# Performance work log

Measured on AMD Instinct MI355X. Metric: run time of the kernel, lower is better.

## Reference

```python
import jax, jax.numpy as jnp
import numpy as np

H = 256      # hidden_dim
NH = 4       # num_heads
DK = H // NH # per-head dim
NL = 2       # num self-attn layers
TL = 6       # transformer_num_layers (output repeat)
PTS_DIM = 3


def _layer_norm(x, g, b, eps=1e-5):
    m = jnp.mean(x, axis=-1, keepdims=True)
    v = jnp.mean((x - m) ** 2, axis=-1, keepdims=True)
    return (x - m) / jnp.sqrt(v + eps) * g + b


def _mha(x, Wq, bq, Wk, bk, Wv, bv, Wo, bo, g, bb, bias):
    # x: [B,N,H]; bias: [B,NH,N,N]; way='add' (att_spm_type='add')
    B, N, _ = x.shape
    q = (x @ Wq + bq).reshape(B, N, NH, DK).transpose(0, 2, 1, 3)  # [B,h,N,d]
    k = (x @ Wk + bk).reshape(B, N, NH, DK).transpose(0, 2, 1, 3)
    v = (x @ Wv + bv).reshape(B, N, NH, DK).transpose(0, 2, 1, 3)
    att = jnp.einsum('bhnd,bhmd->bhnm', q, k) / np.sqrt(DK).astype(np.float32)
    att = jax.nn.softmax(att + bias, axis=-1)
    out = jnp.einsum('bhnm,bhmd->bhnd', att, v).transpose(0, 2, 1, 3).reshape(B, N, H)
    out = out @ Wo + bo
    return _layer_norm(x + out, g, bb)


def setup_inputs() -> dict:
    key = jax.random.key(0)
    ks = jax.random.split(key, 16)
    B, N = 1, 512
    s = 0.02  # weight init scale
    inp = {
        'history_states': jax.random.normal(ks[0], (TL, B, N, H), jnp.float32),
        'all_lanes_preds': jax.random.normal(ks[1], (TL, B, N, 33), jnp.float32),
        'fc_W': jax.random.normal(ks[2], (H, H), jnp.float32) * s,
        'fc_b': jnp.zeros((H,), jnp.float32),
        'Wq': jax.random.normal(ks[3], (NL, H, H), jnp.float32) * s,
        'bq': jnp.zeros((NL, H), jnp.float32),
        'Wk': jax.random.normal(ks[4], (NL, H, H), jnp.float32) * s,
        'bk': jnp.zeros((NL, H), jnp.float32),
        'Wv': jax.random.normal(ks[5], (NL, H, H), jnp.float32) * s,
        'bv': jnp.zeros((NL, H), jnp.float32),
        'Wo': jax.random.normal(ks[6], (NL, H, H), jnp.float32) * s,
        'bo': jnp.zeros((NL, H), jnp.float32),
        'ln_g': jnp.ones((NL, H), jnp.float32),
        'ln_b': jnp.zeros((NL, H), jnp.float32),
        'mlp1_W': jax.random.normal(ks[7], (H, H), jnp.float32) * s,
        'mlp1_b': jnp.zeros((H,), jnp.float32),
        'mlp2_W': jax.random.normal(ks[8], (H, H), jnp.float32) * s,
        'mlp2_b': jnp.zeros((H,), jnp.float32),
        'cls_W1': jax.random.normal(ks[9], (2 * H, H), jnp.float32) * s,
        'cls_b1': jnp.zeros((H,), jnp.float32),
        'cls_W2': jax.random.normal(ks[10], (H, 1), jnp.float32) * s,
        'cls_b2': jnp.zeros((1,), jnp.float32),
    }
    return inp


def reference(history_states, all_lanes_preds, fc_W, fc_b, Wq, bq, Wk, bk, Wv, bv,
              Wo, bo, ln_g, ln_b, mlp1_W, mlp1_b, mlp2_W, mlp2_b,
              cls_W1, cls_b1, cls_W2, cls_b2):
    query_feats = history_states[-1]                 # [B,N,H]
    coords = all_lanes_preds[-1]                      # [B,N,33]
    B, N, C = coords.shape
    coords = coords.reshape(B, N, C // PTS_DIM, PTS_DIM)
    query_end_point = coords[:, :, -1, :]             # [B,N,3]
    key_start_point = coords[:, :, 0, :]              # [B,N,3]

    # pairwise distance bias: dist[b,i,j] = ||key_start[j] - query_end[i]||
    diff = key_start_point[:, None, :, :] - query_end_point[:, :, None, :]
    dist = jnp.sqrt(jnp.sum(diff ** 2, axis=-1))[:, None, :, :]  # [B,1,N,N]
    dw = 1.0 / (dist + 0.01)
    dw = dw / jnp.sum(dw, axis=2, keepdims=True)      # normalize over dim 2
    zeros = jnp.zeros_like(dw)
    dist_weights = jax.lax.stop_gradient(
        jnp.concatenate([dw, -dist, zeros, zeros], axis=1))  # [B,4,N,N]

    # features_concat: Linear + ReLU
    x = jax.nn.relu(query_feats @ fc_W + fc_b)

    for i in range(NL):
        x = _mha(x, Wq[i], bq[i], Wk[i], bk[i], Wv[i], bv[i],
                 Wo[i], bo[i], ln_g[i], ln_b[i], dist_weights)

    # lclc relationship head: per-side MLP, pairwise concat, classifier
    o1 = jax.nn.relu(x @ mlp1_W + mlp1_b)             # [B,N,H]
    o2 = jax.nn.relu(x @ mlp2_W + mlp2_b)
    pair = jnp.concatenate([
        jnp.broadcast_to(o1[:, :, None, :], (B, N, N, H)),
        jnp.broadcast_to(o2[:, None, :, :], (B, N, N, H))], axis=-1)  # [B,N,N,2H]
    z = jax.nn.relu(pair @ cls_W1 + cls_b1)
    lclc = (z @ cls_W2 + cls_b2)[..., 0]              # [B,N,N]
    all_lclc_preds = jnp.broadcast_to(lclc[None], (TL, B, N, N))
    return all_lclc_preds
```

## Files before the change

### kernel.cpp

```cpp
#include <hip/hip_runtime.h>
#include <math.h>


#define NTOK 512
#define HDIM 256
#define DKH  64
#define NHEAD 4
#define TLEN 6
#define WSZ  65536
#define PSTR 520
#define XPS  264

typedef __attribute__((ext_vector_type(8))) short bf16x8;
typedef __attribute__((ext_vector_type(4))) float f32x4;

__device__ __forceinline__ ushort f2bf(float f)
{
    unsigned u = __builtin_bit_cast(unsigned, f);
    u += 0x7FFFu + ((u >> 16) & 1u);
    return (ushort)(u >> 16);
}
__device__ __forceinline__ float bf_lo(unsigned u)
{
    return __builtin_bit_cast(float, u << 16);
}
__device__ __forceinline__ float bf_hi(unsigned u)
{
    return __builtin_bit_cast(float, u & 0xFFFF0000u);
}

struct PKArg {
    const float* w[13];
    const float* pl;
    ushort* wpk;
    float *dist, *dwraw, *inv_cs;
};

__global__ __launch_bounds__(256) void pack_kernel(PKArg p)
{
    __shared__ __align__(16) ushort smu[64 * 72];
    const int bid = blockIdx.x;
    const int t   = threadIdx.x;

    if (bid < 208) {
        const int mat  = bid >> 4;
        const int tile = bid & 15;
        const int k0   = (tile >> 2) * 64;
        const int c0   = (tile & 3) * 64;
        const float* W = p.w[mat];
#pragma unroll
        for (int j = 0; j < 4; ++j) {
            const int i  = t + j * 256;
            const int r  = i >> 4, c4 = i & 15;
            const float4 v4 = *(const float4*)&W[(k0 + r) * HDIM + c0 + c4 * 4];
            smu[(c4 * 4 + 0) * 72 + r] = f2bf(v4.x);
            smu[(c4 * 4 + 1) * 72 + r] = f2bf(v4.y);
            smu[(c4 * 4 + 2) * 72 + r] = f2bf(v4.z);
            smu[(c4 * 4 + 3) * 72 + r] = f2bf(v4.w);
        }
        __syncthreads();
#pragma unroll
        for (int j = 0; j < 2; ++j) {
            const int i  = t + j * 256;
            const int cr = i >> 3, kk = i & 7;
            const uint4 v = *(const uint4*)&smu[cr * 72 + kk * 8];
            *(uint4*)&p.wpk[mat * WSZ + (c0 + cr) * HDIM + k0 + kk * 8] = v;
        }
    } else {
        float* smf = (float*)smu;
        float* qe  = smf;
        float* red = smf + 1536;
        const int item = bid - 208;
        for (int i = t; i < 512; i += 256) {
            qe[i * 3 + 0] = p.pl[i * 33 + 30];
            qe[i * 3 + 1] = p.pl[i * 33 + 31];
            qe[i * 3 + 2] = p.pl[i * 33 + 32];
        }
        __syncthreads();
        const int m   = item * 64 + (t & 63);
        const int nch = t >> 6;
        const float kx = p.pl[m * 33 + 0], ky = p.pl[m * 33 + 1], kz = p.pl[m * 33 + 2];
        float cs = 0.f;
        for (int n = nch * 128; n < nch * 128 + 128; ++n) {
            const float dx = kx - qe[n * 3 + 0];
            const float dy = ky - qe[n * 3 + 1];
            const float dz = kz - qe[n * 3 + 2];
            const float dd = sqrtf(dx * dx + dy * dy + dz * dz);
            const float w  = 1.0f / (dd + 0.01f);
            p.dist[n * NTOK + m]  = dd;
            p.dwraw[n * NTOK + m] = w;
            cs += w;
        }
        red[nch * 64 + (t & 63)] = cs;
        __syncthreads();
        if (t < 64)
            p.inv_cs[item * 64 + t] =
                1.0f / (red[t] + red[64 + t] + red[128 + t] + red[192 + t]);
    }
}

__device__ __forceinline__ void qkv_one2(
    const ushort* __restrict__ xpan, const ushort* __restrict__ Wt,
    const float* __restrict__ bb, int prob,
    int slab, int c0, int lr, int lg, int lk,
    ushort* __restrict__ q16, ushort* __restrict__ k16,
    ushort* __restrict__ vT16)
{
    const ushort* Ap = xpan + lr * XPS + lk;
    f32x4 acc[2];
    acc[0] = (f32x4){0.f, 0.f, 0.f, 0.f};
    acc[1] = (f32x4){0.f, 0.f, 0.f, 0.f};
#pragma unroll
    for (int ks = 0; ks < 8; ++ks) {
        const bf16x8 a = *(const bf16x8*)&Ap[ks * 32];
#pragma unroll
        for (int j = 0; j < 2; ++j) {
            const bf16x8 b = *(const bf16x8*)&Wt[(c0 + j * 16 + lr) * HDIM + ks * 32 + lk];
            acc[j] = __builtin_amdgcn_mfma_f32_16x16x32_bf16(a, b, acc[j], 0, 0, 0);
        }
    }
#pragma unroll
    for (int j = 0; j < 2; ++j) {
        const int col = c0 + j * 16 + lr;
        const float bv2 = bb[col];
        if (prob < 2) {
            ushort* dst = (prob == 0) ? q16 : k16;
#pragma unroll
            for (int rg = 0; rg < 4; ++rg)
                dst[(slab + lg * 4 + rg) * HDIM + col] = f2bf(acc[j][rg] + bv2);
        } else {
            ushort4 s = {f2bf(acc[j][0] + bv2), f2bf(acc[j][1] + bv2),
                         f2bf(acc[j][2] + bv2), f2bf(acc[j][3] + bv2)};
            *(ushort4*)&vT16[col * NTOK + slab + lg * 4] = s;
        }
    }
}

__global__ __launch_bounds__(256) void fcqkv(
    const float* __restrict__ qf, const ushort* __restrict__ fcWt,
    const float* __restrict__ fcb,
    const ushort* __restrict__ WqT, const float* __restrict__ bq,
    const ushort* __restrict__ WkT, const float* __restrict__ bk,
    const ushort* __restrict__ WvT, const float* __restrict__ bv,
    float* __restrict__ xa, ushort* __restrict__ q16,
    ushort* __restrict__ k16, ushort* __restrict__ vT16)
{
    __shared__ __align__(16) ushort xpan[16 * XPS];
    const int bid  = blockIdx.x;
    const int p6   = bid >> 5;
    const int slab = (bid & 31) * 16;
    const int t = threadIdx.x;
    const int wv = t >> 6, lane = t & 63;
    const int lr = lane & 15, lg = lane >> 4, lk = lg * 8;
    const int c0 = wv * 64;

    {
        f32x4 acc[4];
#pragma unroll
        for (int j = 0; j < 4; ++j) acc[j] = (f32x4){0.f, 0.f, 0.f, 0.f};
        const float* Aq = qf + (slab + lr) * HDIM + lk;
#pragma unroll
        for (int ks = 0; ks < 8; ++ks) {
            const float4 a0 = *(const float4*)&Aq[ks * 32];
            const float4 a1 = *(const float4*)&Aq[ks * 32 + 4];
            bf16x8 a;
            a[0] = (short)f2bf(a0.x); a[1] = (short)f2bf(a0.y);
            a[2] = (short)f2bf(a0.z); a[3] = (short)f2bf(a0.w);
            a[4] = (short)f2bf(a1.x); a[5] = (short)f2bf(a1.y);
            a[6] = (short)f2bf(a1.z); a[7] = (short)f2bf(a1.w);
#pragma unroll
            for (int j = 0; j < 4; ++j) {
                const bf16x8 b = *(const bf16x8*)&fcWt[(c0 + j * 16 + lr) * HDIM + ks * 32 + lk];
                acc[j] = __builtin_amdgcn_mfma_f32_16x16x32_bf16(a, b, acc[j], 0, 0, 0);
            }
        }
#pragma unroll
        for (int j = 0; j < 4; ++j) {
            const int col = c0 + j * 16 + lr;
            const float bbv = fcb[col];
#pragma unroll
            for (int rg = 0; rg < 4; ++rg) {
                const float o = fmaxf(acc[j][rg] + bbv, 0.f);
                if (p6 == 0) xa[(slab + lg * 4 + rg) * HDIM + col] = o;
                xpan[(lg * 4 + rg) * XPS + col] = f2bf(o);
            }
        }
    }
    __syncthreads();
    const int prob = p6 >> 1, ch = p6 & 1;
    const ushort* Wt = (prob == 0) ? WqT : (prob == 1) ? WkT : WvT;
    const float*  bb = (prob == 0) ? bq  : (prob == 1) ? bk  : bv;
    qkv_one2(xpan, Wt, bb, prob, slab, ch * 128 + wv * 32, lr, lg, lk,
             q16, k16, vT16);
}

__global__ __launch_bounds__(512) void attn_fused(
    const ushort* __restrict__ q16, const ushort* __restrict__ k16,
    const ushort* __restrict__ vT16, const float* __restrict__ dist,
    const float* __restrict__ dwraw, const float* __restrict__ inv_cs,
    ushort* __restrict__ ao16)
{
    __shared__ __align__(16) ushort P_lds[16 * PSTR];
    __shared__ __align__(16) float exch[2][16][64];
    __shared__ float rmax[8][16];
    __shared__ float psums[8][16];

    const int bid = blockIdx.x;
    const int h  = bid >> 5;
    const int n0 = (bid & 31) * 16;
    const int t  = threadIdx.x;
    const int wv = t >> 6, lane = t & 63;
    const int lr = lane & 15, lg = lane >> 4, lk = lg * 8;
    const int mW = wv * 64;

    const ushort* Qrow = q16 + (n0 + lr) * HDIM + h * DKH + lk;
    const bf16x8 a0 = *(const bf16x8*)&Qrow[0];
    const bf16x8 a1 = *(const bf16x8*)&Qrow[32];

    f32x4 accs[4];
#pragma unroll
    for (int cg = 0; cg < 4; ++cg) accs[cg] = (f32x4){0.f, 0.f, 0.f, 0.f};
#pragma unroll
    for (int cg = 0; cg < 4; ++cg) {
        const ushort* Brow = k16 + (mW + cg * 16 + lr) * HDIM + h * DKH + lk;
        accs[cg] = __builtin_amdgcn_mfma_f32_16x16x32_bf16(
            a0, *(const bf16x8*)&Brow[0], accs[cg], 0, 0, 0);
        accs[cg] = __builtin_amdgcn_mfma_f32_16x16x32_bf16(
            a1, *(const bf16x8*)&Brow[32], accs[cg], 0, 0, 0);
    }

    const int db = wv & 3, kh = wv >> 2;
    const ushort* Vrow = vT16 + (h * DKH + db * 16 + lr) * NTOK + kh * 256 + lk;
    bf16x8 vfrag[8];
#pragma unroll
    for (int c = 0; c < 8; ++c)
        vfrag[c] = *(const bf16x8*)&Vrow[c * 32];

    float s[4][4];
#pragma unroll
    for (int cg = 0; cg < 4; ++cg) {
        const int m = mW + cg * 16 + lr;
        const float ic = (h == 0) ? inv_cs[m] : 0.f;
#pragma unroll
        for (int rg = 0; rg < 4; ++rg) {
            const int n = n0 + lg * 4 + rg;
            float b = 0.f;
            if (h == 0)      b = dwraw[n * NTOK + m] * ic;
            else if (h == 1) b = -dist[n * NTOK + m];
            s[cg][rg] = accs[cg][rg] * 0.125f + b;
        }
    }

    float mx[4];
#pragma unroll
    for (int rg = 0; rg < 4; ++rg) {
        float m = fmaxf(fmaxf(s[0][rg], s[1][rg]), fmaxf(s[2][rg], s[3][rg]));
#pragma unroll
        for (int o = 1; o < 16; o <<= 1) m = fmaxf(m, __shfl_xor(m, o));
        mx[rg] = m;
    }
    if (lr == 0)
#pragma unroll
        for (int rg = 0; rg < 4; ++rg) rmax[wv][lg * 4 + rg] = mx[rg];
    __syncthreads();
    float mxf[4];
#pragma unroll
    for (int rg = 0; rg < 4; ++rg) {
        const int row = lg * 4 + rg;
        float m = rmax[0][row];
#pragma unroll
        for (int w = 1; w < 8; ++w) m = fmaxf(m, rmax[w][row]);
        mxf[rg] = m;
    }

    float ps[4] = {0.f, 0.f, 0.f, 0.f};
#pragma unroll
    for (int cg = 0; cg < 4; ++cg)
#pragma unroll
        for (int rg = 0; rg < 4; ++rg) {
            const float e = __expf(s[cg][rg] - mxf[rg]);
            ps[rg] += e;
            P_lds[(lg * 4 + rg) * PSTR + mW + cg * 16 + lr] = f2bf(e);
        }
#pragma unroll
    for (int rg = 0; rg < 4; ++rg) {
#pragma unroll
        for (int o = 1; o < 16; o <<= 1) ps[rg] += __shfl_xor(ps[rg], o);
    }
    if (lr == 0)
#pragma unroll
        for (int rg = 0; rg < 4; ++rg) psums[wv][lg * 4 + rg] = ps[rg];
    __syncthreads();

    {
        f32x4 acco = (f32x4){0.f, 0.f, 0.f, 0.f};
        const ushort* Prow = P_lds + lr * PSTR + kh * 256 + lk;
#pragma unroll
        for (int c = 0; c < 8; ++c) {
            const bf16x8 pa = *(const bf16x8*)&Prow[c * 32];
            acco = __builtin_amdgcn_mfma_f32_16x16x32_bf16(pa, vfrag[c], acco, 0, 0, 0);
        }
#pragma unroll
        for (int rg = 0; rg < 4; ++rg)
            exch[kh][lg * 4 + rg][db * 16 + lr] = acco[rg];
    }
    __syncthreads();

    if (t < 256) {
        const int r = t >> 4, d4 = t & 15;
        f32x4 sum = *(const f32x4*)&exch[0][r][d4 * 4];
        sum += *(const f32x4*)&exch[1][r][d4 * 4];
        float den = 0.f;
#pragma unroll
        for (int w = 0; w < 8; ++w) den += psums[w][r];
        const float inv = 1.0f / den;
        ushort4 o = {f2bf(sum.x * inv), f2bf(sum.y * inv),
                     f2bf(sum.z * inv), f2bf(sum.w * inv)};
        *(ushort4*)&ao16[(n0 + r) * HDIM + h * DKH + d4 * 4] = o;
    }
}

__device__ __forceinline__ void oprojln_phase(
    const ushort* __restrict__ ao16, const ushort* __restrict__ WoT,
    const float* __restrict__ bo, const float* __restrict__ gamma,
    const float* __restrict__ beta, const float* __restrict__ x,
    int slab, int c0, int wv, int lr, int lg, int lk,
    float red[4][16], f32x4 acc[4])
{
    const ushort* Arow = ao16 + (slab + lr) * HDIM + lk;
#pragma unroll
    for (int j = 0; j < 4; ++j) acc[j] = (f32x4){0.f, 0.f, 0.f, 0.f};
#pragma unroll
    for (int ks = 0; ks < 8; ++ks) {
        const bf16x8 a = *(const bf16x8*)&Arow[ks * 32];
#pragma unroll
        for (int j = 0; j < 4; ++j) {
            const bf16x8 b = *(const bf16x8*)&WoT[(c0 + j * 16 + lr) * HDIM + ks * 32 + lk];
            acc[j] = __builtin_amdgcn_mfma_f32_16x16x32_bf16(a, b, acc[j], 0, 0, 0);
        }
    }
#pragma unroll
    for (int j = 0; j < 4; ++j) {
        const int col = c0 + j * 16 + lr;
        const float bc = bo[col];
#pragma unroll
        for (int rg = 0; rg < 4; ++rg)
            acc[j][rg] += bc + x[(slab + lg * 4 + rg) * HDIM + col];
    }

    float sm[4];
#pragma unroll
    for (int rg = 0; rg < 4; ++rg) {
        float s = 0.f;
#pragma unroll
        for (int j = 0; j < 4; ++j) s += acc[j][rg];
#pragma unroll
        for (int o = 1; o < 16; o <<= 1) s += __shfl_xor(s, o);
        sm[rg] = s;
    }
    if (lr == 0)
#pragma unroll
        for (int rg = 0; rg < 4; ++rg) red[wv][lg * 4 + rg] = sm[rg];
    __syncthreads();
    float mean[4];
#pragma unroll
    for (int rg = 0; rg < 4; ++rg) {
        const int row = lg * 4 + rg;
        mean[rg] = (red[0][row] + red[1][row] + red[2][row] + red[3][row]) * (1.f / 256.f);
    }
    __syncthreads();

#pragma unroll
    for (int rg = 0; rg < 4; ++rg) {
        float s2 = 0.f;
#pragma unroll
        for (int j = 0; j < 4; ++j) {
            const float c = acc[j][rg] - mean[rg];
            s2 += c * c;
        }
#pragma unroll
        for (int o = 1; o < 16; o <<= 1) s2 += __shfl_xor(s2, o);
        sm[rg] = s2;
    }
    if (lr == 0)
#pragma unroll
        for (int rg = 0; rg < 4; ++rg) red[wv][lg * 4 + rg] = sm[rg];
    __syncthreads();
    float rstd[4];
#pragma unroll
    for (int rg = 0; rg < 4; ++rg) {
        const int row = lg * 4 + rg;
        const float var = (red[0][row] + red[1][row] + red[2][row] + red[3][row]) * (1.f / 256.f);
        rstd[rg] = rsqrtf(var + 1e-5f);
    }
#pragma unroll
    for (int j = 0; j < 4; ++j) {
        const int col = c0 + j * 16 + lr;
        const float gg = gamma[col], bv = beta[col];
#pragma unroll
        for (int rg = 0; rg < 4; ++rg)
            acc[j][rg] = (acc[j][rg] - mean[rg]) * rstd[rg] * gg + bv;
    }
}

__global__ __launch_bounds__(256) void oprojqkv(
    const ushort* __restrict__ ao16, const ushort* __restrict__ WoT,
    const float* __restrict__ bo, const float* __restrict__ gamma,
    const float* __restrict__ beta,
    const ushort* __restrict__ WqT, const float* __restrict__ bq,
    const ushort* __restrict__ WkT, const float* __restrict__ bk,
    const ushort* __restrict__ WvT, const float* __restrict__ bv,
    const float* __restrict__ xa, float* __restrict__ xb,
    ushort* __restrict__ q16, ushort* __restrict__ k16,
    ushort* __restrict__ vT16)
{
    __shared__ __align__(16) ushort xpan[16 * XPS];
    __shared__ float red[4][16];
    const int bid  = blockIdx.x;
    const int p6   = bid >> 5;
    const int slab = (bid & 31) * 16;
    const int t = threadIdx.x;
    const int wv = t >> 6, lane = t & 63;
    const int lr = lane & 15, lg = lane >> 4, lk = lg * 8;
    const int c0 = wv * 64;

    f32x4 acc[4];
    oprojln_phase(ao16, WoT, bo, gamma, beta, xa, slab, c0, wv, lr, lg, lk, red, acc);
#pragma unroll
    for (int j = 0; j < 4; ++j) {
        const int col = c0 + j * 16 + lr;
#pragma unroll
        for (int rg = 0; rg < 4; ++rg) {
            if (p6 == 0) xb[(slab + lg * 4 + rg) * HDIM + col] = acc[j][rg];
            xpan[(lg * 4 + rg) * XPS + col] = f2bf(acc[j][rg]);
        }
    }
    __syncthreads();
    const int prob = p6 >> 1, ch = p6 & 1;
    const ushort* Wt = (prob == 0) ? WqT : (prob == 1) ? WkT : WvT;
    const float*  bb = (prob == 0) ? bq  : (prob == 1) ? bk  : bv;
    qkv_one2(xpan, Wt, bb, prob, slab, ch * 128 + wv * 32, lr, lg, lk,
             q16, k16, vT16);
}

__global__ __launch_bounds__(256) void oprojmlpU(
    const ushort* __restrict__ ao16, const ushort* __restrict__ WoT,
    const float* __restrict__ bo, const float* __restrict__ gamma,
    const float* __restrict__ beta,
    const ushort* __restrict__ m1WT, const float* __restrict__ m1b,
    const ushort* __restrict__ m2WT, const float* __restrict__ m2b,
    const ushort* __restrict__ cW1aT, const float* __restrict__ cb1,
    const ushort* __restrict__ cW1bT,
    const float* __restrict__ xb, ushort* __restrict__ U1b,
    ushort* __restrict__ U2b)
{
    __shared__ __align__(16) ushort xpan[16 * XPS];
    __shared__ __align__(16) ushort opan[16 * XPS];
    __shared__ float red[4][16];
    const int bid  = blockIdx.x;
    const int p4   = bid >> 5;
    const int p    = p4 >> 1, ch = p4 & 1;
    const int slab = (bid & 31) * 16;
    const int t = threadIdx.x;
    const int wv = t >> 6, lane = t & 63;
    const int lr = lane & 15, lg = lane >> 4, lk = lg * 8;
    const int c0 = wv * 64;

    f32x4 acc[4];
    oprojln_phase(ao16, WoT, bo, gamma, beta, xb, slab, c0, wv, lr, lg, lk, red, acc);
#pragma unroll
    for (int j = 0; j < 4; ++j) {
        const int col = c0 + j * 16 + lr;
#pragma unroll
        for (int rg = 0; rg < 4; ++rg)
            xpan[(lg * 4 + rg) * XPS + col] = f2bf(acc[j][rg]);
    }
    __syncthreads();

    {
        const ushort* Wt = p ? m2WT : m1WT;
        const float*  bb = p ? m2b  : m1b;
        const ushort* Ap = xpan + lr * XPS + lk;
        f32x4 a2[4];
#pragma unroll
        for (int j = 0; j < 4; ++j) a2[j] = (f32x4){0.f, 0.f, 0.f, 0.f};
#pragma unroll
        for (int ks = 0; ks < 8; ++ks) {
            const bf16x8 a = *(const bf16x8*)&Ap[ks * 32];
#pragma unroll
            for (int j = 0; j < 4; ++j) {
                const bf16x8 b = *(const bf16x8*)&Wt[(c0 + j * 16 + lr) * HDIM + ks * 32 + lk];
                a2[j] = __builtin_amdgcn_mfma_f32_16x16x32_bf16(a, b, a2[j], 0, 0, 0);
            }
        }
#pragma unroll
        for (int j = 0; j < 4; ++j) {
            const int col = c0 + j * 16 + lr;
            const float bbv = bb[col];
#pragma unroll
            for (int rg = 0; rg < 4; ++rg)
                opan[(lg * 4 + rg) * XPS + col] = f2bf(fmaxf(a2[j][rg] + bbv, 0.f));
        }
    }
    __syncthreads();

    {
        const ushort* Wt = p ? cW1bT : cW1aT;
        ushort* U        = p ? U2b : U1b;
        const int cb     = ch * 128 + wv * 32;
        const ushort* Ao = opan + lr * XPS + lk;
        f32x4 a2[2];
        a2[0] = (f32x4){0.f, 0.f, 0.f, 0.f};
        a2[1] = (f32x4){0.f, 0.f, 0.f, 0.f};
#pragma unroll
        for (int ks = 0; ks < 8; ++ks) {
            const bf16x8 a = *(const bf16x8*)&Ao[ks * 32];
#pragma unroll
            for (int j = 0; j < 2; ++j) {
                const bf16x8 b = *(const bf16x8*)&Wt[(cb + j * 16 + lr) * HDIM + ks * 32 + lk];
                a2[j] = __builtin_amdgcn_mfma_f32_16x16x32_bf16(a, b, a2[j], 0, 0, 0);
            }
        }
#pragma unroll
        for (int j = 0; j < 2; ++j) {
            const int col = cb + j * 16 + lr;
            const float bbv = (p == 0) ? cb1[col] : 0.f;
#pragma unroll
            for (int rg = 0; rg < 4; ++rg)
                U[(slab + lg * 4 + rg) * HDIM + col] = f2bf(a2[j][rg] + bbv);
        }
    }
}

__global__ __launch_bounds__(256) void pair_cls(const ushort* __restrict__ U1b,
                                                const ushort* __restrict__ U2b,
                                                const float* __restrict__ W2,
                                                const float* __restrict__ b2,
                                                float* __restrict__ out)
{
    __shared__ __align__(16) ushort u1s[32][264];
    __shared__ __align__(16) ushort u2s[32][264];
    __shared__ __align__(16) float w2s[256];
    const int t  = threadIdx.x;
    const int n0 = blockIdx.y * 32, m0 = blockIdx.x * 32;

#pragma unroll
    for (int u = 0; u < 4; ++u) {
        const int i = t + u * 256;
        const int r = i >> 5, c8 = i & 31;
        *(uint4*)&u1s[r][c8 * 8] = *(const uint4*)&U1b[(n0 + r) * HDIM + c8 * 8];
        *(uint4*)&u2s[r][c8 * 8] = *(const uint4*)&U2b[(m0 + r) * HDIM + c8 * 8];
    }
    if (t < 64) *(float4*)&w2s[t * 4] = *(const float4*)&W2[t * 4];
    __syncthreads();

    const int tx = t & 15, ty = t >> 4;
    const ushort* r0 = &u1s[ty * 2][0];
    const ushort* r1 = &u1s[ty * 2 + 1][0];
    const ushort* c0 = &u2s[tx * 2][0];
    const ushort* c1 = &u2s[tx * 2 + 1][0];
    float acc[2][2] = {};

#define RT(A, B) fmaxf((A) + (B), 0.f)
    for (int h8 = 0; h8 < 32; ++h8) {
        const uint4 A0 = *(const uint4*)&r0[h8 * 8];
        const uint4 A1 = *(const uint4*)&r1[h8 * 8];
        const uint4 B0 = *(const uint4*)&c0[h8 * 8];
        const uint4 B1 = *(const uint4*)&c1[h8 * 8];
        const float4 w0 = *(const float4*)&w2s[h8 * 8];
        const float4 w1 = *(const float4*)&w2s[h8 * 8 + 4];
        const float warr[8] = {w0.x, w0.y, w0.z, w0.w, w1.x, w1.y, w1.z, w1.w};
#pragma unroll
        for (int q = 0; q < 4; ++q) {
            const unsigned a0u = ((const unsigned*)&A0)[q];
            const unsigned a1u = ((const unsigned*)&A1)[q];
            const unsigned b0u = ((const unsigned*)&B0)[q];
            const unsigned b1u = ((const unsigned*)&B1)[q];
            const float a0l = bf_lo(a0u), a0h = bf_hi(a0u);
            const float a1l = bf_lo(a1u), a1h = bf_hi(a1u);
            const float b0l = bf_lo(b0u), b0h = bf_hi(b0u);
            const float b1l = bf_lo(b1u), b1h = bf_hi(b1u);
            const float wl = warr[q * 2], wh = warr[q * 2 + 1];
            acc[0][0] += RT(a0l, b0l) * wl + RT(a0h, b0h) * wh;
            acc[0][1] += RT(a0l, b1l) * wl + RT(a0h, b1h) * wh;
            acc[1][0] += RT(a1l, b0l) * wl + RT(a1h, b0h) * wh;
            acc[1][1] += RT(a1l, b1l) * wl + RT(a1h, b1h) * wh;
        }
    }
#undef RT

    const float bbv = b2[0];
#pragma unroll
    for (int ii = 0; ii < 2; ++ii)
#pragma unroll
        for (int jj = 0; jj < 2; ++jj) {
            const float val = acc[ii][jj] + bbv;
            const int n = n0 + ty * 2 + ii;
            const int m = m0 + tx * 2 + jj;
#pragma unroll
            for (int tl = 0; tl < TLEN; ++tl)
                out[tl * NTOK * NTOK + n * NTOK + m] = val;
        }
}

extern "C" void kernel_launch(void* const* d_in, const int* in_sizes, int n_in,
                              void* d_out, int out_size, void* d_ws, size_t ws_size,
                              hipStream_t stream)
{
    const float* hs   = (const float*)d_in[0];
    const float* qf   = hs + 5 * NTOK * HDIM;
    const float* alp  = (const float*)d_in[1];
    const float* pl   = alp + 5 * NTOK * 33;
    const float* fc_W = (const float*)d_in[2];
    const float* fc_b = (const float*)d_in[3];
    const float* Wq   = (const float*)d_in[4];
    const float* bq   = (const float*)d_in[5];
    const float* Wk   = (const float*)d_in[6];
    const float* bk   = (const float*)d_in[7];
    const float* Wv   = (const float*)d_in[8];
    const float* bv   = (const float*)d_in[9];
    const float* Wo   = (const float*)d_in[10];
    const float* bo   = (const float*)d_in[11];
    const float* lng  = (const float*)d_in[12];
    const float* lnb  = (const float*)d_in[13];
    const float* m1W  = (const float*)d_in[14];
    const float* m1b  = (const float*)d_in[15];
    const float* m2W  = (const float*)d_in[16];
    const float* m2b  = (const float*)d_in[17];
    const float* cW1  = (const float*)d_in[18];
    const float* cb1  = (const float*)d_in[19];
    const float* cW2  = (const float*)d_in[20];
    const float* cb2  = (const float*)d_in[21];
    float* out = (float*)d_out;

    const int NN  = NTOK * NTOK;
    const int NH_ = NTOK * HDIM;
    float* ws     = (float*)d_ws;
    float* dist   = ws;
    float* dwraw  = ws + NN;
    float* inv_cs = ws + 2 * NN;
    float* xa     = ws + 2 * NN + 512;
    float* xb     = xa + NH_;
    ushort* u16   = (ushort*)(xb + NH_);
    ushort* wpk   = u16;
    ushort* q16   = wpk + 13 * WSZ;
    ushort* k16   = q16 + NH_;
    ushort* vT16  = k16 + NH_;
    ushort* ao16  = vT16 + NH_;
    ushort* U1b   = ao16 + NH_;
    ushort* U2b   = U1b + NH_;

    PKArg pk;
    pk.w[0]  = fc_W;
    pk.w[1]  = Wq;  pk.w[2]  = Wq + WSZ;
    pk.w[3]  = Wk;  pk.w[4]  = Wk + WSZ;
    pk.w[5]  = Wv;  pk.w[6]  = Wv + WSZ;
    pk.w[7]  = Wo;  pk.w[8]  = Wo + WSZ;
    pk.w[9]  = m1W; pk.w[10] = m2W;
    pk.w[11] = cW1; pk.w[12] = cW1 + WSZ;
    pk.pl = pl;
    pk.wpk = wpk;
    pk.dist = dist; pk.dwraw = dwraw; pk.inv_cs = inv_cs;
    pack_kernel<<<216, 256, 0, stream>>>(pk);

    fcqkv<<<192, 256, 0, stream>>>(
        qf, wpk + 0 * WSZ, fc_b,
        wpk + 1 * WSZ, bq, wpk + 3 * WSZ, bk, wpk + 5 * WSZ, bv,
        xa, q16, k16, vT16);

    attn_fused<<<128, 512, 0, stream>>>(q16, k16, vT16, dist, dwraw, inv_cs, ao16);

    oprojqkv<<<192, 256, 0, stream>>>(
        ao16, wpk + 7 * WSZ, bo, lng, lnb,
        wpk + 2 * WSZ, bq + HDIM, wpk + 4 * WSZ, bk + HDIM,
        wpk + 6 * WSZ, bv + HDIM,
        xa, xb, q16, k16, vT16);

    attn_fused<<<128, 512, 0, stream>>>(q16, k16, vT16, dist, dwraw, inv_cs, ao16);

    oprojmlpU<<<128, 256, 0, stream>>>(
        ao16, wpk + 8 * WSZ, bo + HDIM, lng + HDIM, lnb + HDIM,
        wpk + 9 * WSZ, m1b, wpk + 10 * WSZ, m2b,
        wpk + 11 * WSZ, cb1, wpk + 12 * WSZ,
        xb, U1b, U2b);

    pair_cls<<<dim3(16, 16), 256, 0, stream>>>(U1b, U2b, cW2, cb2, out);
}
```

Measured before the change: 95.28 us.

## Split weight packing so only first-layer weights precede fcqkv, overlap rest

```diff
diff --git a/kernel.cpp b/kernel.cpp
--- a/kernel.cpp
+++ b/kernel.cpp
@@ -29,74 +29,73 @@
     return __builtin_bit_cast(float, u & 0xFFFF0000u);
 }
 
-struct PKArg {
-    const float* w[13];
-    const float* pl;
-    ushort* wpk;
-    float *dist, *dwraw, *inv_cs;
-};
-
-__global__ __launch_bounds__(256) void pack_kernel(PKArg p)
+__device__ void pack_tile(const float* __restrict__ W, ushort* __restrict__ dst,
+                          int tile, ushort* smu)
+{
+    const int k0 = (tile >> 2) * 64;
+    const int c0 = (tile & 3) * 64;
+    const int t  = threadIdx.x;
+#pragma unroll
+    for (int j = 0; j < 4; ++j) {
+        const int i  = t + j * 256;
+        const int r  = i >> 4, c4 = i & 15;
+        const float4 v4 = *(const float4*)&W[(k0 + r) * HDIM + c0 + c4 * 4];
+        smu[(c4 * 4 + 0) * 72 + r] = f2bf(v4.x);
+        smu[(c4 * 4 + 1) * 72 + r] = f2bf(v4.y);
+        smu[(c4 * 4 + 2) * 72 + r] = f2bf(v4.z);
+        smu[(c4 * 4 + 3) * 72 + r] = f2bf(v4.w);
+    }
+    __syncthreads();
+#pragma unroll
+    for (int j = 0; j < 2; ++j) {
+        const int i  = t + j * 256;
+        const int cr = i >> 3, kk = i & 7;
+        const uint4 v = *(const uint4*)&smu[cr * 72 + kk * 8];
+        *(uint4*)&dst[(c0 + cr) * HDIM + k0 + kk * 8] = v;
+    }
+}
+
+__device__ void dist_item(const float* __restrict__ pl, float* __restrict__ dist,
+                          float* __restrict__ dwraw, float* __restrict__ inv_cs,
+                          int item, float* smf)
+{
+    float* qe  = smf;
+    float* red = smf + 1536;
+    const int t = threadIdx.x;
+    for (int i = t; i < 512; i += 256) {
+        qe[i * 3 + 0] = pl[i * 33 + 30];
+        qe[i * 3 + 1] = pl[i * 33 + 31];
+        qe[i * 3 + 2] = pl[i * 33 + 32];
+    }
+    __syncthreads();
+    const int m   = item * 64 + (t & 63);
+    const int nch = t >> 6;
+    const float kx = pl[m * 33 + 0], ky = pl[m * 33 + 1], kz = pl[m * 33 + 2];
+    float cs = 0.f;
+    for (int n = nch * 128; n < nch * 128 + 128; ++n) {
+        const float dx = kx - qe[n * 3 + 0];
+        const float dy = ky - qe[n * 3 + 1];
+        const float dz = kz - qe[n * 3 + 2];
+        const float dd = sqrtf(dx * dx + dy * dy + dz * dz);
+        const float w  = 1.0f / (dd + 0.01f);
+        dist[n * NTOK + m]  = dd;
+        dwraw[n * NTOK + m] = w;
+        cs += w;
+    }
+    red[nch * 64 + (t & 63)] = cs;
+    __syncthreads();
+    if (t < 64)
+        inv_cs[item * 64 + t] =
+            1.0f / (red[t] + red[64 + t] + red[128 + t] + red[192 + t]);
+}
+
+struct PK1 { const float* w[4]; int mat[4]; ushort* wpk; };
+
+__global__ __launch_bounds__(256) void pack1_kernel(PK1 p)
 {
     __shared__ __align__(16) ushort smu[64 * 72];
-    const int bid = blockIdx.x;
-    const int t   = threadIdx.x;
-
-    if (bid < 208) {
-        const int mat  = bid >> 4;
-        const int tile = bid & 15;
-        const int k0   = (tile >> 2) * 64;
-        const int c0   = (tile & 3) * 64;
-        const float* W = p.w[mat];
-#pragma unroll
-        for (int j = 0; j < 4; ++j) {
-            const int i  = t + j * 256;
-            const int r  = i >> 4, c4 = i & 15;
-            const float4 v4 = *(const float4*)&W[(k0 + r) * HDIM + c0 + c4 * 4];
-            smu[(c4 * 4 + 0) * 72 + r] = f2bf(v4.x);
-            smu[(c4 * 4 + 1) * 72 + r] = f2bf(v4.y);
-            smu[(c4 * 4 + 2) * 72 + r] = f2bf(v4.z);
-            smu[(c4 * 4 + 3) * 72 + r] = f2bf(v4.w);
-        }
-        __syncthreads();
-#pragma unroll
-        for (int j = 0; j < 2; ++j) {
-            const int i  = t + j * 256;
-            const int cr = i >> 3, kk = i & 7;
-            const uint4 v = *(const uint4*)&smu[cr * 72 + kk * 8];
-            *(uint4*)&p.wpk[mat * WSZ + (c0 + cr) * HDIM + k0 + kk * 8] = v;
-        }
-    } else {
-        float* smf = (float*)smu;
-        float* qe  = smf;
-        float* red = smf + 1536;
-        const int item = bid - 208;
-        for (int i = t; i < 512; i += 256) {
-            qe[i * 3 + 0] = p.pl[i * 33 + 30];
-            qe[i * 3 + 1] = p.pl[i * 33 + 31];
-            qe[i * 3 + 2] = p.pl[i * 33 + 32];
-        }
-        __syncthreads();
-        const int m   = item * 64 + (t & 63);
-        const int nch = t >> 6;
-        const float kx = p.pl[m * 33 + 0], ky = p.pl[m * 33 + 1], kz = p.pl[m * 33 + 2];
-        float cs = 0.f;
-        for (int n = nch * 128; n < nch * 128 + 128; ++n) {
-            const float dx = kx - qe[n * 3 + 0];
-            const float dy = ky - qe[n * 3 + 1];
-            const float dz = kz - qe[n * 3 + 2];
-            const float dd = sqrtf(dx * dx + dy * dy + dz * dz);
-            const float w  = 1.0f / (dd + 0.01f);
-            p.dist[n * NTOK + m]  = dd;
-            p.dwraw[n * NTOK + m] = w;
-            cs += w;
-        }
-        red[nch * 64 + (t & 63)] = cs;
-        __syncthreads();
-        if (t < 64)
-            p.inv_cs[item * 64 + t] =
-                1.0f / (red[t] + red[64 + t] + red[128 + t] + red[192 + t]);
-    }
+    const int mi = blockIdx.x >> 4;
+    pack_tile(p.w[mi], p.wpk + p.mat[mi] * WSZ, blockIdx.x & 15, smu);
 }
 
 __device__ __forceinline__ void qkv_one2(
@@ -135,6 +134,8 @@
         }
     }
 }
+
+struct FQAux { const float* w[9]; int mat[9]; };
 
 __global__ __launch_bounds__(256) void fcqkv(
     const float* __restrict__ qf, const ushort* __restrict__ fcWt,
@@ -143,10 +144,25 @@
     const ushort* __restrict__ WkT, const float* __restrict__ bk,
     const ushort* __restrict__ WvT, const float* __restrict__ bv,
     float* __restrict__ xa, ushort* __restrict__ q16,
-    ushort* __restrict__ k16, ushort* __restrict__ vT16)
-{
-    __shared__ __align__(16) ushort xpan[16 * XPS];
+    ushort* __restrict__ k16, ushort* __restrict__ vT16,
+    FQAux aux, ushort* __restrict__ wpk, const float* __restrict__ pl,
+    float* __restrict__ dist, float* __restrict__ dwraw,
+    float* __restrict__ inv_cs)
+{
+    __shared__ __align__(16) ushort smu[64 * 72];
     const int bid  = blockIdx.x;
+
+    if (bid >= 192) {
+        const int ib = bid - 192;
+        if (ib < 144) {
+            pack_tile(aux.w[ib >> 4], wpk + aux.mat[ib >> 4] * WSZ, ib & 15, smu);
+        } else {
+            dist_item(pl, dist, dwraw, inv_cs, ib - 144, (float*)smu);
+        }
+        return;
+    }
+
+    ushort* xpan = smu;
     const int p6   = bid >> 5;
     const int slab = (bid & 31) * 16;
     const int t = threadIdx.x;
@@ -650,23 +666,30 @@
     ushort* U1b   = ao16 + NH_;
     ushort* U2b   = U1b + NH_;
 
-    PKArg pk;
-    pk.w[0]  = fc_W;
-    pk.w[1]  = Wq;  pk.w[2]  = Wq + WSZ;
-    pk.w[3]  = Wk;  pk.w[4]  = Wk + WSZ;
-    pk.w[5]  = Wv;  pk.w[6]  = Wv + WSZ;
-    pk.w[7]  = Wo;  pk.w[8]  = Wo + WSZ;
-    pk.w[9]  = m1W; pk.w[10] = m2W;
-    pk.w[11] = cW1; pk.w[12] = cW1 + WSZ;
-    pk.pl = pl;
-    pk.wpk = wpk;
-    pk.dist = dist; pk.dwraw = dwraw; pk.inv_cs = inv_cs;
-    pack_kernel<<<216, 256, 0, stream>>>(pk);
-
-    fcqkv<<<192, 256, 0, stream>>>(
+    PK1 p1;
+    p1.w[0] = fc_W; p1.mat[0] = 0;
+    p1.w[1] = Wq;   p1.mat[1] = 1;
+    p1.w[2] = Wk;   p1.mat[2] = 3;
+    p1.w[3] = Wv;   p1.mat[3] = 5;
+    p1.wpk = wpk;
+    pack1_kernel<<<64, 256, 0, stream>>>(p1);
+
+    FQAux aux;
+    aux.w[0] = Wq + WSZ;        aux.mat[0] = 2;
+    aux.w[1] = Wk + WSZ;        aux.mat[1] = 4;
+    aux.w[2] = Wv + WSZ;        aux.mat[2] = 6;
+    aux.w[3] = Wo;              aux.mat[3] = 7;
+    aux.w[4] = Wo + WSZ;        aux.mat[4] = 8;
+    aux.w[5] = m1W;             aux.mat[5] = 9;
+    aux.w[6] = m2W;             aux.mat[6] = 10;
+    aux.w[7] = cW1;             aux.mat[7] = 11;
+    aux.w[8] = cW1 + WSZ;       aux.mat[8] = 12;
+
+    fcqkv<<<344, 256, 0, stream>>>(
         qf, wpk + 0 * WSZ, fc_b,
         wpk + 1 * WSZ, bq, wpk + 3 * WSZ, bk, wpk + 5 * WSZ, bv,
-        xa, q16, k16, vT16);
+        xa, q16, k16, vT16,
+        aux, wpk, pl, dist, dwraw, inv_cs);
 
     attn_fused<<<128, 512, 0, stream>>>(q16, k16, vT16, dist, dwraw, inv_cs, ao16);
 
```

Result: faster. 92.50 us, median of 2 (-2.9%).
